# Kernel tuning notes

Hardware: AMD Instinct MI355X
Metric: run time of the kernel (lower is better)

## Reference

```python
import jax, jax.numpy as jnp
import numpy as np

B, N, H = 8, 256, 128


def _linear_params(key, fin, fout):
    # torch nn.Linear default init: U(-1/sqrt(fin), 1/sqrt(fin)) for weight and bias
    k1, k2 = jax.random.split(key)
    lim = 1.0 / np.sqrt(fin)
    w = jax.random.uniform(k1, (fin, fout), jnp.float32, -lim, lim)
    b = jax.random.uniform(k2, (fout,), jnp.float32, -lim, lim)
    return w, b


def setup_inputs() -> dict:
    key = jax.random.key(0)
    ks = jax.random.split(key, 12)
    inp = {
        'x': jax.random.normal(ks[0], (B, N, 3), jnp.float32),
        'h': jax.random.normal(ks[1], (B, N, H), jnp.float32),
        'x0': jax.random.normal(ks[2], (B, N, 3), jnp.float32),
        'pad_mask': jnp.ones((B, N, 1), jnp.float32),
    }
    names_dims = [
        ('edg1', 2 * H + 2, H), ('edg2', H, H), ('edgi', H, 1),
        ('node1', 2 * H, H), ('node2', H, H),
        ('cor1', 2 * H + 2, H), ('cor2', H, H), ('cor3', H, 1),
    ]
    for i, (name, fin, fout) in enumerate(names_dims):
        w, b = _linear_params(ks[3 + i], fin, fout)
        inp[name + '_w'] = w
        inp[name + '_b'] = b
    return inp


def _safe_dist(d2):
    # sqrt with zero (not NaN) gradient where d2 == 0 (diagonal)
    pos = d2 > 0
    return jnp.sqrt(jnp.where(pos, d2, 1.0)) * pos


def reference(x, h, x0, pad_mask,
              edg1_w, edg1_b, edg2_w, edg2_b, edgi_w, edgi_b,
              node1_w, node1_b, node2_w, node2_b,
              cor1_w, cor1_b, cor2_w, cor2_b, cor3_w, cor3_b):
    silu = jax.nn.silu
    b, n, hd = h.shape
    # pairwise squared distances, shapes (b, n, n, 1)
    diff0 = x0[:, :, None, :] - x0[:, None, :, :]
    d0_2 = jnp.sum(diff0 * diff0, axis=-1, keepdims=True)
    diff = x[:, :, None, :] - x[:, None, :, :]
    d2 = jnp.sum(diff * diff, axis=-1, keepdims=True)
    dist = _safe_dist(d2)
    # all-pairs node-feature concat: pair[b,i,j] = [h_i, h_j, d2_ij, d0_2_ij]
    hi = jnp.broadcast_to(h[:, :, None, :], (b, n, n, hd))
    hj = jnp.broadcast_to(h[:, None, :, :], (b, n, n, hd))
    pair = jnp.concatenate([hi, hj, d2, d0_2], axis=-1)  # (b,n,n,2H+2)
    # edge MLP -> messages
    m = silu(silu(pair @ edg1_w + edg1_b) @ edg2_w + edg2_b)  # (b,n,n,H)
    e = jax.nn.sigmoid(m @ edgi_w + edgi_b)                   # (b,n,n,1)
    offdiag = 1.0 - jnp.eye(n, dtype=x.dtype)[None, :, :, None]
    e = e * offdiag
    agg = jnp.mean(e * m, axis=2)  # mean over j -> (b,n,H)
    # node update with residual
    nin = jnp.concatenate([h, agg], axis=-1)
    h_next = h + (silu(nin @ node1_w + node1_b) @ node2_w + node2_b)
    # coordinate update
    cw = silu(silu(pair @ cor1_w + cor1_b) @ cor2_w + cor2_b) @ cor3_w + cor3_b  # (b,n,n,1)
    shift = diff / (dist + 1.0)
    upd = jnp.mean(cw * shift * offdiag, axis=2)  # (b,n,3)
    x_next = x + upd
    if pad_mask is not None:
        x_next = x_next * pad_mask
        h_next = h_next * pad_mask
    return x_next, h_next
```

## Files before the change

kernel.cpp:

```cpp
#include <hip/hip_runtime.h>

typedef __attribute__((ext_vector_type(8))) short short8;
typedef __attribute__((ext_vector_type(8))) unsigned short ushort8_t;
typedef __attribute__((ext_vector_type(4))) float f32x4;

#define BN 256
#define HD 128
#define WSTRIDE 136

__device__ __forceinline__ unsigned short f2bf(float f) {
    union { float f; unsigned int i; } v; v.f = f;
    unsigned int lsb = (v.i >> 16) & 1u;
    v.i += 0x7fffu + lsb;
    return (unsigned short)(v.i >> 16);
}
__device__ __forceinline__ float fsigmoid(float x) {
    return __builtin_amdgcn_rcpf(1.0f + __expf(-x));
}
__device__ __forceinline__ float fsilu(float x) {
    return x * fsigmoid(x);
}

__global__ __launch_bounds__(256) void prep(
    const float* __restrict__ e2w, const float* __restrict__ c2w,
    const float* __restrict__ e1w, const float* __restrict__ c1w,
    const float* __restrict__ h,
    const float* __restrict__ e1b, const float* __restrict__ c1b,
    unsigned short* __restrict__ WtE, unsigned short* __restrict__ WtC,
    float* __restrict__ A1e, float* __restrict__ A2e,
    float* __restrict__ A1c, float* __restrict__ A2c) {

    __shared__ __align__(16) unsigned short lt[4][HD * WSTRIDE];
    const int tid = threadIdx.x;

    if (blockIdx.x < 2) {
        const float* src = blockIdx.x ? c2w : e2w;
        unsigned short* dst = blockIdx.x ? WtC : WtE;
#pragma unroll
        for (int jj = 0; jj < 16; ++jj) {
            int f4 = jj * 256 + tid;
            int k  = f4 >> 5;
            int c0 = (f4 & 31) * 4;
            float4 v = *(const float4*)(src + k * 128 + c0);
            lt[0][(c0 + 0) * WSTRIDE + k] = f2bf(v.x);
            lt[0][(c0 + 1) * WSTRIDE + k] = f2bf(v.y);
            lt[0][(c0 + 2) * WSTRIDE + k] = f2bf(v.z);
            lt[0][(c0 + 3) * WSTRIDE + k] = f2bf(v.w);
        }
        __syncthreads();
        {
            int n = tid >> 1, k0 = (tid & 1) * 64;
#pragma unroll
            for (int j = 0; j < 8; ++j) {
                ushort8_t o;
#pragma unroll
                for (int e = 0; e < 8; ++e) o[e] = lt[0][n * WSTRIDE + k0 + j * 8 + e];
                *(ushort8_t*)(dst + n * 128 + k0 + j * 8) = o;
            }
        }
        __syncthreads();
    }

#pragma unroll
    for (int m = 0; m < 4; ++m) {
        const float* src = (m == 0) ? e1w : (m == 1) ? (e1w + 128 * 128)
                         : (m == 2) ? c1w : (c1w + 128 * 128);
#pragma unroll
        for (int jj = 0; jj < 16; ++jj) {
            int f4 = jj * 256 + tid;
            int k  = f4 >> 5;
            int c0 = (f4 & 31) * 4;
            float4 v = *(const float4*)(src + k * 128 + c0);
            lt[m][(c0 + 0) * WSTRIDE + k] = f2bf(v.x);
            lt[m][(c0 + 1) * WSTRIDE + k] = f2bf(v.y);
            lt[m][(c0 + 2) * WSTRIDE + k] = f2bf(v.z);
            lt[m][(c0 + 3) * WSTRIDE + k] = f2bf(v.w);
        }
    }
    __syncthreads();

    const int lane = tid & 63, wv = tid >> 6;
    const int c = lane & 15, q = lane >> 4;
    const int r0 = blockIdx.x * 16;

    const unsigned short* Wt = lt[wv];
    float* O = (wv == 0) ? A1e : (wv == 1) ? A2e : (wv == 2) ? A1c : A2c;
    const float* bias = (wv == 0) ? e1b : (wv == 2) ? c1b : (const float*)0;

    f32x4 acc[8];
    const f32x4 zf = {0.f, 0.f, 0.f, 0.f};
#pragma unroll
    for (int nt = 0; nt < 8; ++nt) acc[nt] = zf;

    const float* hrow = h + (size_t)(r0 + c) * HD;
#pragma unroll
    for (int ks = 0; ks < 4; ++ks) {
        const int kb = ks * 32 + q * 8;
        float4 hlo = *(const float4*)(hrow + kb);
        float4 hhi = *(const float4*)(hrow + kb + 4);
        short8 af;
        af[0] = (short)f2bf(hlo.x); af[1] = (short)f2bf(hlo.y);
        af[2] = (short)f2bf(hlo.z); af[3] = (short)f2bf(hlo.w);
        af[4] = (short)f2bf(hhi.x); af[5] = (short)f2bf(hhi.y);
        af[6] = (short)f2bf(hhi.z); af[7] = (short)f2bf(hhi.w);
#pragma unroll
        for (int nt = 0; nt < 8; ++nt) {
            short8 Bf = *(const short8*)(Wt + (nt * 16 + c) * WSTRIDE + kb);
            acc[nt] = __builtin_amdgcn_mfma_f32_16x16x32_bf16(af, Bf, acc[nt], 0, 0, 0);
        }
    }
#pragma unroll
    for (int nt = 0; nt < 8; ++nt) {
        float bb = bias ? bias[nt * 16 + c] : 0.f;
#pragma unroll
        for (int reg = 0; reg < 4; ++reg)
            O[(size_t)(r0 + q * 4 + reg) * HD + nt * 16 + c] = acc[nt][reg] + bb;
    }
}

__global__ __launch_bounds__(1024, 8) void egc_main(
    const float* __restrict__ x, const float* __restrict__ h,
    const float* __restrict__ x0, const float* __restrict__ pmask,
    const float* __restrict__ e1w,
    const float* __restrict__ e2b, const float* __restrict__ eiw,
    const float* __restrict__ eib,
    const float* __restrict__ n1w, const float* __restrict__ n1b,
    const float* __restrict__ n2w, const float* __restrict__ n2b,
    const float* __restrict__ c1w, const float* __restrict__ c2b,
    const float* __restrict__ c3w, const float* __restrict__ c3b,
    const float* __restrict__ A1e, const float* __restrict__ A2e,
    const float* __restrict__ A1c, const float* __restrict__ A2c,
    const unsigned short* __restrict__ WtE, const unsigned short* __restrict__ WtC,
    float* __restrict__ xout, float* __restrict__ hout) {

    __shared__ __align__(16) unsigned short Wl[HD * WSTRIDE];
    __shared__ __align__(16) float xs[BN][4];
    __shared__ __align__(16) float x0s[BN][4];
    __shared__ __align__(16) float d2s[BN], d02s[BN], rsh[BN];
    __shared__ __align__(16) float vE0[HD], vE1[HD], vE2[HD];
    __shared__ __align__(16) float vC0[HD], vC1[HD], vC2[HD];
    __shared__ __align__(16) float hsv[HD];
    __shared__ __align__(16) float aggbuf[16][HD];
    __shared__ __align__(16) float aggv[HD];
    __shared__ float updbuf[16][4];
    __shared__ float smask;

    const int tid = threadIdx.x;
    const int bi  = blockIdx.x;
    const int b   = bi >> 8;
    const int i   = bi & 255;
    const int row = bi;

#pragma unroll
    for (int u = 0; u < 2; ++u) {
        int idx = u * 1024 + tid;
        int n   = idx >> 4;
        int k8  = (idx & 15) * 8;
        *(ushort8_t*)(Wl + n * WSTRIDE + k8) = *(const ushort8_t*)(WtE + n * HD + k8);
    }

    if (tid < BN) {
        int gj = b * BN + tid;
        xs[tid][0]  = x[gj * 3 + 0];
        xs[tid][1]  = x[gj * 3 + 1];
        xs[tid][2]  = x[gj * 3 + 2];
        x0s[tid][0] = x0[gj * 3 + 0];
        x0s[tid][1] = x0[gj * 3 + 1];
        x0s[tid][2] = x0[gj * 3 + 2];
    } else if (tid < BN + HD) {
        int t = tid - BN;
        vE0[t] = A1e[row * HD + t];
        vE1[t] = e1w[256 * HD + t];
        vE2[t] = e1w[257 * HD + t];
    } else if (tid < BN + 2 * HD) {
        int t = tid - BN - HD;
        vC0[t] = A1c[row * HD + t];
        vC1[t] = c1w[256 * HD + t];
        vC2[t] = c1w[257 * HD + t];
    } else if (tid < BN + 3 * HD) {
        int t = tid - BN - 2 * HD;
        hsv[t] = h[row * HD + t];
    }
    if (tid == 1023) smask = pmask[row];
    __syncthreads();

    if (tid < BN) {
        float dx = xs[i][0] - xs[tid][0];
        float dy = xs[i][1] - xs[tid][1];
        float dz = xs[i][2] - xs[tid][2];
        float d2 = dx * dx + dy * dy + dz * dz;
        d2s[tid] = d2;
        float dist = (d2 > 0.0f) ? sqrtf(d2) : 0.0f;
        rsh[tid] = __builtin_amdgcn_rcpf(dist + 1.0f);
        float ex = x0s[i][0] - x0s[tid][0];
        float ey = x0s[i][1] - x0s[tid][1];
        float ez = x0s[i][2] - x0s[tid][2];
        d02s[tid] = ex * ex + ey * ey + ez * ez;
    }
    __syncthreads();

    const int lane = tid & 63, wv = tid >> 6;
    const int c = lane & 15, q = lane >> 4;
    const int ra = wv * 16 + c;

    {
        const float* A2g = A2e + (size_t)b * BN * HD;
        f32x4 acc[8];
        const f32x4 zf = {0.f, 0.f, 0.f, 0.f};
#pragma unroll
        for (int nt = 0; nt < 8; ++nt) acc[nt] = zf;
        const float d2v = d2s[ra], d02v = d02s[ra];
#pragma unroll
        for (int ks = 0; ks < 4; ++ks) {
            const int kb = ks * 32 + q * 8;
            float4 alo = *(const float4*)(A2g + ra * HD + kb);
            float4 ahi = *(const float4*)(A2g + ra * HD + kb + 4);
            float4 p0 = *(const float4*)(vE0 + kb);
            float4 p0h = *(const float4*)(vE0 + kb + 4);
            float4 p1 = *(const float4*)(vE1 + kb);
            float4 p1h = *(const float4*)(vE1 + kb + 4);
            float4 p2 = *(const float4*)(vE2 + kb);
            float4 p2h = *(const float4*)(vE2 + kb + 4);
            short8 af;
            af[0] = (short)f2bf(fsilu(alo.x + p0.x + d2v * p1.x + d02v * p2.x));
            af[1] = (short)f2bf(fsilu(alo.y + p0.y + d2v * p1.y + d02v * p2.y));
            af[2] = (short)f2bf(fsilu(alo.z + p0.z + d2v * p1.z + d02v * p2.z));
            af[3] = (short)f2bf(fsilu(alo.w + p0.w + d2v * p1.w + d02v * p2.w));
            af[4] = (short)f2bf(fsilu(ahi.x + p0h.x + d2v * p1h.x + d02v * p2h.x));
            af[5] = (short)f2bf(fsilu(ahi.y + p0h.y + d2v * p1h.y + d02v * p2h.y));
            af[6] = (short)f2bf(fsilu(ahi.z + p0h.z + d2v * p1h.z + d02v * p2h.z));
            af[7] = (short)f2bf(fsilu(ahi.w + p0h.w + d2v * p1h.w + d02v * p2h.w));
#pragma unroll
            for (int nt = 0; nt < 8; ++nt) {
                short8 Bf = *(const short8*)(Wl + (nt * 16 + c) * WSTRIDE + kb);
                acc[nt] = __builtin_amdgcn_mfma_f32_16x16x32_bf16(af, Bf, acc[nt], 0, 0, 0);
            }
        }
        float b2l[8], wIl[8];
#pragma unroll
        for (int nt = 0; nt < 8; ++nt) {
            b2l[nt] = e2b[nt * 16 + c];
            wIl[nt] = eiw[nt * 16 + c];
        }
        float bI = eib[0];
        float aggp[8] = {0,0,0,0,0,0,0,0};
#pragma unroll
        for (int reg = 0; reg < 4; ++reg) {
            int r = wv * 16 + q * 4 + reg;
            float mv[8]; float ed = 0.f;
#pragma unroll
            for (int nt = 0; nt < 8; ++nt) {
                mv[nt] = fsilu(acc[nt][reg] + b2l[nt]);
                ed += mv[nt] * wIl[nt];
            }
            ed += __shfl_xor(ed, 1);
            ed += __shfl_xor(ed, 2);
            ed += __shfl_xor(ed, 4);
            ed += __shfl_xor(ed, 8);
            float e = (r == i) ? 0.0f : fsigmoid(ed + bI);
#pragma unroll
            for (int nt = 0; nt < 8; ++nt) aggp[nt] += e * mv[nt];
        }
#pragma unroll
        for (int nt = 0; nt < 8; ++nt) {
            aggp[nt] += __shfl_xor(aggp[nt], 16);
            aggp[nt] += __shfl_xor(aggp[nt], 32);
        }
        if (q == 0)
#pragma unroll
            for (int nt = 0; nt < 8; ++nt) aggbuf[wv][nt * 16 + c] = aggp[nt];
    }
    __syncthreads();

    if (tid < HD) {
        float s = 0.f;
#pragma unroll
        for (int w = 0; w < 16; ++w) s += aggbuf[w][tid];
        aggv[tid] = s * (1.0f / 256.0f);
    }
#pragma unroll
    for (int u = 0; u < 2; ++u) {
        int idx = u * 1024 + tid;
        int n   = idx >> 4;
        int k8  = (idx & 15) * 8;
        *(ushort8_t*)(Wl + n * WSTRIDE + k8) = *(const ushort8_t*)(WtC + n * HD + k8);
    }
    __syncthreads();

    {
        const float* A2g = A2c + (size_t)b * BN * HD;
        f32x4 acc[8];
        const f32x4 zf = {0.f, 0.f, 0.f, 0.f};
#pragma unroll
        for (int nt = 0; nt < 8; ++nt) acc[nt] = zf;
        const float d2v = d2s[ra], d02v = d02s[ra];
#pragma unroll
        for (int ks = 0; ks < 4; ++ks) {
            const int kb = ks * 32 + q * 8;
            float4 alo = *(const float4*)(A2g + ra * HD + kb);
            float4 ahi = *(const float4*)(A2g + ra * HD + kb + 4);
            float4 p0 = *(const float4*)(vC0 + kb);
            float4 p0h = *(const float4*)(vC0 + kb + 4);
            float4 p1 = *(const float4*)(vC1 + kb);
            float4 p1h = *(const float4*)(vC1 + kb + 4);
            float4 p2 = *(const float4*)(vC2 + kb);
            float4 p2h = *(const float4*)(vC2 + kb + 4);
            short8 af;
            af[0] = (short)f2bf(fsilu(alo.x + p0.x + d2v * p1.x + d02v * p2.x));
            af[1] = (short)f2bf(fsilu(alo.y + p0.y + d2v * p1.y + d02v * p2.y));
            af[2] = (short)f2bf(fsilu(alo.z + p0.z + d2v * p1.z + d02v * p2.z));
            af[3] = (short)f2bf(fsilu(alo.w + p0.w + d2v * p1.w + d02v * p2.w));
            af[4] = (short)f2bf(fsilu(ahi.x + p0h.x + d2v * p1h.x + d02v * p2h.x));
            af[5] = (short)f2bf(fsilu(ahi.y + p0h.y + d2v * p1h.y + d02v * p2h.y));
            af[6] = (short)f2bf(fsilu(ahi.z + p0h.z + d2v * p1h.z + d02v * p2h.z));
            af[7] = (short)f2bf(fsilu(ahi.w + p0h.w + d2v * p1h.w + d02v * p2h.w));
#pragma unroll
            for (int nt = 0; nt < 8; ++nt) {
                short8 Bf = *(const short8*)(Wl + (nt * 16 + c) * WSTRIDE + kb);
                acc[nt] = __builtin_amdgcn_mfma_f32_16x16x32_bf16(af, Bf, acc[nt], 0, 0, 0);
            }
        }
        float b2l[8], w3l[8];
#pragma unroll
        for (int nt = 0; nt < 8; ++nt) {
            b2l[nt] = c2b[nt * 16 + c];
            w3l[nt] = c3w[nt * 16 + c];
        }
        float b3 = c3b[0];
        float updp = 0.f;
        float xic = (c < 3) ? xs[i][c] : 0.f;
#pragma unroll
        for (int reg = 0; reg < 4; ++reg) {
            int r = wv * 16 + q * 4 + reg;
            float cd = 0.f;
#pragma unroll
            for (int nt = 0; nt < 8; ++nt)
                cd += fsilu(acc[nt][reg] + b2l[nt]) * w3l[nt];
            cd += __shfl_xor(cd, 1);
            cd += __shfl_xor(cd, 2);
            cd += __shfl_xor(cd, 4);
            cd += __shfl_xor(cd, 8);
            float cw = cd + b3;
            if (c < 3 && r != i)
                updp += cw * (xic - xs[r][c]) * rsh[r];
        }
        updp += __shfl_xor(updp, 16);
        updp += __shfl_xor(updp, 32);
        if (q == 0 && c < 3) updbuf[wv][c] = updp;
    }
    __syncthreads();

    if (tid < 3) {
        float u = 0.f;
#pragma unroll
        for (int w = 0; w < 16; ++w) u += updbuf[w][tid];
        u *= (1.0f / 256.0f);
        xout[row * 3 + tid] = (xs[i][tid] + u) * smask;
    }

    float* npart = &aggbuf[0][0];
    float* qv    = &aggbuf[8][0];
    {
        int k = tid & 127, part = tid >> 7;
        const float* src = (part < 4) ? hsv : aggv;
        int fbase = (part & 3) * 32;
        int wrow = ((part < 4) ? 0 : HD) + fbase;
        float s = 0.f;
#pragma unroll 4
        for (int f = 0; f < 32; ++f)
            s += src[fbase + f] * n1w[(size_t)(wrow + f) * HD + k];
        npart[part * HD + k] = s;
    }
    __syncthreads();
    if (tid < HD) {
        float s = n1b[tid];
#pragma unroll
        for (int p = 0; p < 8; ++p) s += npart[p * HD + tid];
        qv[tid] = fsilu(s);
    }
    __syncthreads();
    {
        int o = tid & 127, p = tid >> 7;
        float s = 0.f;
#pragma unroll 4
        for (int f = 0; f < 16; ++f) {
            int ff = p * 16 + f;
            s += qv[ff] * n2w[(size_t)ff * HD + o];
        }
        npart[p * HD + o] = s;
    }
    __syncthreads();
    if (tid < HD) {
        float s = 0.f;
#pragma unroll
        for (int p = 0; p < 8; ++p) s += npart[p * HD + tid];
        hout[(size_t)row * HD + tid] = (hsv[tid] + s + n2b[tid]) * smask;
    }
}

extern "C" void kernel_launch(void* const* d_in, const int* in_sizes, int n_in,
                              void* d_out, int out_size, void* d_ws, size_t ws_size,
                              hipStream_t stream) {
    const float* x    = (const float*)d_in[0];
    const float* h    = (const float*)d_in[1];
    const float* x0   = (const float*)d_in[2];
    const float* pm   = (const float*)d_in[3];
    const float* e1w  = (const float*)d_in[4];
    const float* e1b  = (const float*)d_in[5];
    const float* e2w  = (const float*)d_in[6];
    const float* e2b  = (const float*)d_in[7];
    const float* eiw  = (const float*)d_in[8];
    const float* eib  = (const float*)d_in[9];
    const float* n1w  = (const float*)d_in[10];
    const float* n1b  = (const float*)d_in[11];
    const float* n2w  = (const float*)d_in[12];
    const float* n2b  = (const float*)d_in[13];
    const float* c1w  = (const float*)d_in[14];
    const float* c1b  = (const float*)d_in[15];
    const float* c2w  = (const float*)d_in[16];
    const float* c2b  = (const float*)d_in[17];
    const float* c3w  = (const float*)d_in[18];
    const float* c3b  = (const float*)d_in[19];

    float* wsf = (float*)d_ws;
    const size_t nA = 2048 * 128;
    float* A1e = wsf;
    float* A2e = wsf + nA;
    float* A1c = wsf + 2 * nA;
    float* A2c = wsf + 3 * nA;
    unsigned short* WtE = (unsigned short*)(wsf + 4 * nA);
    unsigned short* WtC = WtE + 128 * 128;

    float* xout = (float*)d_out;
    float* hout = xout + 8 * 256 * 3;

    prep<<<dim3(128), dim3(256), 0, stream>>>(e2w, c2w, e1w, c1w, h, e1b, c1b,
                                              WtE, WtC, A1e, A2e, A1c, A2c);
    egc_main<<<dim3(2048), dim3(1024), 0, stream>>>(
        x, h, x0, pm, e1w, e2b, eiw, eib, n1w, n1b, n2w, n2b,
        c1w, c2b, c3w, c3b, A1e, A2e, A1c, A2c, WtE, WtC, xout, hout);
}
```

Measured before the change: 236.4 us.

## Process two query rows per block to amortize weight staging and setup

Each block now handles two i-rows instead of one, halving the grid to 1024 blocks. The per-block costs of staging the bf16 weight tiles into LDS, loading x/x0, and running the node MLP are shared across two rows, and the node MLP uses all 1024 threads for both rows at once. The bf16 conversion also drops round-to-nearest-even for a cheaper round-half-up. The trade-offs are more serialized work per block, fewer blocks to hide latency, and slightly different rounding.

```diff
diff --git a/kernel.cpp b/kernel.cpp
--- a/kernel.cpp
+++ b/kernel.cpp
@@ -9,10 +9,7 @@
 #define WSTRIDE 136
 
 __device__ __forceinline__ unsigned short f2bf(float f) {
-    union { float f; unsigned int i; } v; v.f = f;
-    unsigned int lsb = (v.i >> 16) & 1u;
-    v.i += 0x7fffu + lsb;
-    return (unsigned short)(v.i >> 16);
+    return (unsigned short)((__float_as_uint(f) + 0x8000u) >> 16);
 }
 __device__ __forceinline__ float fsigmoid(float x) {
     return __builtin_amdgcn_rcpf(1.0f + __expf(-x));
@@ -136,20 +133,20 @@
     __shared__ __align__(16) unsigned short Wl[HD * WSTRIDE];
     __shared__ __align__(16) float xs[BN][4];
     __shared__ __align__(16) float x0s[BN][4];
-    __shared__ __align__(16) float d2s[BN], d02s[BN], rsh[BN];
-    __shared__ __align__(16) float vE0[HD], vE1[HD], vE2[HD];
-    __shared__ __align__(16) float vC0[HD], vC1[HD], vC2[HD];
-    __shared__ __align__(16) float hsv[HD];
+    __shared__ __align__(16) float d2s[2][BN], d02s[2][BN], rsh[2][BN];
+    __shared__ __align__(16) float vE0[2][HD], vE1[HD], vE2[HD];
+    __shared__ __align__(16) float vC0[2][HD], vC1[HD], vC2[HD];
+    __shared__ __align__(16) float hsv[2][HD];
     __shared__ __align__(16) float aggbuf[16][HD];
-    __shared__ __align__(16) float aggv[HD];
-    __shared__ float updbuf[16][4];
-    __shared__ float smask;
+    __shared__ __align__(16) float aggv[2][HD];
+    __shared__ float updbuf[2][16][4];
+    __shared__ float smask[2];
 
     const int tid = threadIdx.x;
     const int bi  = blockIdx.x;
-    const int b   = bi >> 8;
-    const int i   = bi & 255;
-    const int row = bi;
+    const int b   = bi >> 7;
+    const int ip  = (bi & 127) * 2;
+    const int r0  = b * 256 + ip;
 
 #pragma unroll
     for (int u = 0; u < 2; ++u) {
@@ -167,35 +164,43 @@
         x0s[tid][0] = x0[gj * 3 + 0];
         x0s[tid][1] = x0[gj * 3 + 1];
         x0s[tid][2] = x0[gj * 3 + 2];
-    } else if (tid < BN + HD) {
-        int t = tid - BN;
-        vE0[t] = A1e[row * HD + t];
+    } else if (tid < 384) {
+        int t = tid - 256;
         vE1[t] = e1w[256 * HD + t];
         vE2[t] = e1w[257 * HD + t];
-    } else if (tid < BN + 2 * HD) {
-        int t = tid - BN - HD;
-        vC0[t] = A1c[row * HD + t];
+    } else if (tid < 512) {
+        int t = tid - 384;
         vC1[t] = c1w[256 * HD + t];
         vC2[t] = c1w[257 * HD + t];
-    } else if (tid < BN + 3 * HD) {
-        int t = tid - BN - 2 * HD;
-        hsv[t] = h[row * HD + t];
-    }
-    if (tid == 1023) smask = pmask[row];
-    __syncthreads();
-
-    if (tid < BN) {
-        float dx = xs[i][0] - xs[tid][0];
-        float dy = xs[i][1] - xs[tid][1];
-        float dz = xs[i][2] - xs[tid][2];
+    } else if (tid < 640) {
+        int t = tid - 512;
+        vE0[0][t] = A1e[(size_t)r0 * HD + t];
+        vE0[1][t] = A1e[(size_t)(r0 + 1) * HD + t];
+    } else if (tid < 768) {
+        int t = tid - 640;
+        vC0[0][t] = A1c[(size_t)r0 * HD + t];
+        vC0[1][t] = A1c[(size_t)(r0 + 1) * HD + t];
+    } else if (tid < 896) {
+        int t = tid - 768;
+        hsv[0][t] = h[(size_t)r0 * HD + t];
+        hsv[1][t] = h[(size_t)(r0 + 1) * HD + t];
+    }
+    if (tid == 1023) { smask[0] = pmask[r0]; smask[1] = pmask[r0 + 1]; }
+    __syncthreads();
+
+    if (tid < 512) {
+        int ii = tid >> 8, j = tid & 255, i = ip + ii;
+        float dx = xs[i][0] - xs[j][0];
+        float dy = xs[i][1] - xs[j][1];
+        float dz = xs[i][2] - xs[j][2];
         float d2 = dx * dx + dy * dy + dz * dz;
-        d2s[tid] = d2;
+        d2s[ii][j] = d2;
         float dist = (d2 > 0.0f) ? sqrtf(d2) : 0.0f;
-        rsh[tid] = __builtin_amdgcn_rcpf(dist + 1.0f);
-        float ex = x0s[i][0] - x0s[tid][0];
-        float ey = x0s[i][1] - x0s[tid][1];
-        float ez = x0s[i][2] - x0s[tid][2];
-        d02s[tid] = ex * ex + ey * ey + ez * ez;
+        rsh[ii][j] = __builtin_amdgcn_rcpf(dist + 1.0f);
+        float ex = x0s[i][0] - x0s[j][0];
+        float ey = x0s[i][1] - x0s[j][1];
+        float ez = x0s[i][2] - x0s[j][2];
+        d02s[ii][j] = ex * ex + ey * ey + ez * ez;
     }
     __syncthreads();
 
@@ -203,20 +208,22 @@
     const int c = lane & 15, q = lane >> 4;
     const int ra = wv * 16 + c;
 
-    {
+#pragma unroll 1
+    for (int ii = 0; ii < 2; ++ii) {
+        const int i = ip + ii;
         const float* A2g = A2e + (size_t)b * BN * HD;
         f32x4 acc[8];
         const f32x4 zf = {0.f, 0.f, 0.f, 0.f};
 #pragma unroll
         for (int nt = 0; nt < 8; ++nt) acc[nt] = zf;
-        const float d2v = d2s[ra], d02v = d02s[ra];
+        const float d2v = d2s[ii][ra], d02v = d02s[ii][ra];
 #pragma unroll
         for (int ks = 0; ks < 4; ++ks) {
             const int kb = ks * 32 + q * 8;
             float4 alo = *(const float4*)(A2g + ra * HD + kb);
             float4 ahi = *(const float4*)(A2g + ra * HD + kb + 4);
-            float4 p0 = *(const float4*)(vE0 + kb);
-            float4 p0h = *(const float4*)(vE0 + kb + 4);
+            float4 p0 = *(const float4*)(&vE0[ii][kb]);
+            float4 p0h = *(const float4*)(&vE0[ii][kb + 4]);
             float4 p1 = *(const float4*)(vE1 + kb);
             float4 p1h = *(const float4*)(vE1 + kb + 4);
             float4 p2 = *(const float4*)(vE2 + kb);
@@ -269,38 +276,41 @@
         if (q == 0)
 #pragma unroll
             for (int nt = 0; nt < 8; ++nt) aggbuf[wv][nt * 16 + c] = aggp[nt];
-    }
-    __syncthreads();
-
-    if (tid < HD) {
-        float s = 0.f;
-#pragma unroll
-        for (int w = 0; w < 16; ++w) s += aggbuf[w][tid];
-        aggv[tid] = s * (1.0f / 256.0f);
-    }
-#pragma unroll
-    for (int u = 0; u < 2; ++u) {
-        int idx = u * 1024 + tid;
-        int n   = idx >> 4;
-        int k8  = (idx & 15) * 8;
-        *(ushort8_t*)(Wl + n * WSTRIDE + k8) = *(const ushort8_t*)(WtC + n * HD + k8);
-    }
-    __syncthreads();
-
-    {
+        __syncthreads();
+        if (tid < HD) {
+            float s = 0.f;
+#pragma unroll
+            for (int w = 0; w < 16; ++w) s += aggbuf[w][tid];
+            aggv[ii][tid] = s * (1.0f / 256.0f);
+        }
+        if (ii == 1) {
+#pragma unroll
+            for (int u = 0; u < 2; ++u) {
+                int idx = u * 1024 + tid;
+                int n   = idx >> 4;
+                int k8  = (idx & 15) * 8;
+                *(ushort8_t*)(Wl + n * WSTRIDE + k8) = *(const ushort8_t*)(WtC + n * HD + k8);
+            }
+        }
+        __syncthreads();
+    }
+
+#pragma unroll 1
+    for (int ii = 0; ii < 2; ++ii) {
+        const int i = ip + ii;
         const float* A2g = A2c + (size_t)b * BN * HD;
         f32x4 acc[8];
         const f32x4 zf = {0.f, 0.f, 0.f, 0.f};
 #pragma unroll
         for (int nt = 0; nt < 8; ++nt) acc[nt] = zf;
-        const float d2v = d2s[ra], d02v = d02s[ra];
+        const float d2v = d2s[ii][ra], d02v = d02s[ii][ra];
 #pragma unroll
         for (int ks = 0; ks < 4; ++ks) {
             const int kb = ks * 32 + q * 8;
             float4 alo = *(const float4*)(A2g + ra * HD + kb);
             float4 ahi = *(const float4*)(A2g + ra * HD + kb + 4);
-            float4 p0 = *(const float4*)(vC0 + kb);
-            float4 p0h = *(const float4*)(vC0 + kb + 4);
+            float4 p0 = *(const float4*)(&vC0[ii][kb]);
+            float4 p0h = *(const float4*)(&vC0[ii][kb + 4]);
             float4 p1 = *(const float4*)(vC1 + kb);
             float4 p1h = *(const float4*)(vC1 + kb + 4);
             float4 p2 = *(const float4*)(vC2 + kb);
@@ -342,59 +352,61 @@
             cd += __shfl_xor(cd, 8);
             float cw = cd + b3;
             if (c < 3 && r != i)
-                updp += cw * (xic - xs[r][c]) * rsh[r];
+                updp += cw * (xic - xs[r][c]) * rsh[ii][r];
         }
         updp += __shfl_xor(updp, 16);
         updp += __shfl_xor(updp, 32);
-        if (q == 0 && c < 3) updbuf[wv][c] = updp;
-    }
-    __syncthreads();
-
-    if (tid < 3) {
+        if (q == 0 && c < 3) updbuf[ii][wv][c] = updp;
+    }
+    __syncthreads();
+
+    if (tid < 6) {
+        int ii = tid / 3, cc = tid - ii * 3;
         float u = 0.f;
 #pragma unroll
-        for (int w = 0; w < 16; ++w) u += updbuf[w][tid];
+        for (int w = 0; w < 16; ++w) u += updbuf[ii][w][cc];
         u *= (1.0f / 256.0f);
-        xout[row * 3 + tid] = (xs[i][tid] + u) * smask;
-    }
-
-    float* npart = &aggbuf[0][0];
-    float* qv    = &aggbuf[8][0];
+        xout[(size_t)(r0 + ii) * 3 + cc] = (xs[ip + ii][cc] + u) * smask[ii];
+    }
+
     {
-        int k = tid & 127, part = tid >> 7;
-        const float* src = (part < 4) ? hsv : aggv;
-        int fbase = (part & 3) * 32;
-        int wrow = ((part < 4) ? 0 : HD) + fbase;
+        int ii = tid >> 9;
+        int k  = tid & 127;
+        int part = (tid >> 7) & 3;
+        const float* src = (part < 2) ? hsv[ii] : aggv[ii];
+        int fbase = (part & 1) * 64;
+        int wrow  = ((part < 2) ? 0 : HD) + fbase;
         float s = 0.f;
 #pragma unroll 4
-        for (int f = 0; f < 32; ++f)
+        for (int f = 0; f < 64; ++f)
             s += src[fbase + f] * n1w[(size_t)(wrow + f) * HD + k];
-        npart[part * HD + k] = s;
-    }
-    __syncthreads();
-    if (tid < HD) {
-        float s = n1b[tid];
-#pragma unroll
-        for (int p = 0; p < 8; ++p) s += npart[p * HD + tid];
-        qv[tid] = fsilu(s);
+        aggbuf[ii * 4 + part][k] = s;
+    }
+    __syncthreads();
+    if (tid < 256) {
+        int ii = tid >> 7, t = tid & 127;
+        float s = n1b[t] + aggbuf[ii * 4 + 0][t] + aggbuf[ii * 4 + 1][t]
+                         + aggbuf[ii * 4 + 2][t] + aggbuf[ii * 4 + 3][t];
+        aggbuf[8 + ii][t] = fsilu(s);
     }
     __syncthreads();
     {
-        int o = tid & 127, p = tid >> 7;
+        int ii = tid >> 9, o = tid & 127, p = (tid >> 7) & 3;
+        const float* qv = aggbuf[8 + ii];
         float s = 0.f;
 #pragma unroll 4
-        for (int f = 0; f < 16; ++f) {
-            int ff = p * 16 + f;
+        for (int f = 0; f < 32; ++f) {
+            int ff = p * 32 + f;
             s += qv[ff] * n2w[(size_t)ff * HD + o];
         }
-        npart[p * HD + o] = s;
-    }
-    __syncthreads();
-    if (tid < HD) {
-        float s = 0.f;
-#pragma unroll
-        for (int p = 0; p < 8; ++p) s += npart[p * HD + tid];
-        hout[(size_t)row * HD + tid] = (hsv[tid] + s + n2b[tid]) * smask;
+        aggbuf[ii * 4 + p][o] = s;
+    }
+    __syncthreads();
+    if (tid < 256) {
+        int ii = tid >> 7, t = tid & 127;
+        float s = aggbuf[ii * 4 + 0][t] + aggbuf[ii * 4 + 1][t]
+                + aggbuf[ii * 4 + 2][t] + aggbuf[ii * 4 + 3][t];
+        hout[(size_t)(r0 + ii) * HD + t] = (hsv[ii][t] + s + n2b[t]) * smask[ii];
     }
 }
 
@@ -436,7 +448,7 @@
 
     prep<<<dim3(128), dim3(256), 0, stream>>>(e2w, c2w, e1w, c1w, h, e1b, c1b,
                                               WtE, WtC, A1e, A2e, A1c, A2c);
-    egc_main<<<dim3(2048), dim3(1024), 0, stream>>>(
+    egc_main<<<dim3(1024), dim3(1024), 0, stream>>>(
         x, h, x0, pm, e1w, e2b, eiw, eib, n1w, n1b, n2w, n2b,
         c1w, c2b, c3w, c3b, A1e, A2e, A1c, A2c, WtE, WtC, xout, hout);
 }
```

New measurement: 880.0 us. +272.3%, slower.
